# Kernel optimization log

Hardware: AMD Instinct MI355X
Metric: run time of the kernel (lower is better)

Reference implementation:

```python
import jax, jax.numpy as jnp
import numpy as np

EPS = 1e-6
ALPHA = 0.2  # LeakyReLU negative slope


def layer_norm(x, g, b):
    mu = jnp.mean(x, axis=-1, keepdims=True)
    var = jnp.mean(jnp.square(x - mu), axis=-1, keepdims=True)
    return (x - mu) * jax.lax.rsqrt(var + EPS) * g + b


def graph_attention(x, bias, W, a_src, a_dst):
    # x: [B,N,D], bias: [B,N,N], W: [D, H*Dh], a_src/a_dst: [H, Dh]
    B, N, D = x.shape
    H, Dh = a_src.shape
    h = jnp.einsum('bnd,dhk->bhnk', x, W.reshape(D, H, Dh))  # [B,H,N,Dh]
    s = jnp.einsum('bhnk,hk->bhn', h, a_src)                 # source term
    t = jnp.einsum('bhnk,hk->bhn', h, a_dst)                 # target term
    e = jax.nn.leaky_relu(s[:, :, :, None] + t[:, :, None, :], ALPHA)
    e = e + bias[:, None, :, :]                              # graph mask/bias
    attn = jax.nn.softmax(e, axis=-1)                        # [B,H,N,N]
    out = jnp.einsum('bhij,bhjk->bhik', attn, h)             # [B,H,N,Dh]
    return out.transpose(0, 2, 1, 3).reshape(B, N, H * Dh)


def setup_inputs() -> dict:
    key = jax.random.key(0)
    ks = jax.random.split(key, 8)
    B, N, D, H = 2, 2048, 512, 8
    Dh = D // H
    sc = 1.0 / np.sqrt(D)
    return {
        'x': jax.random.normal(ks[0], (B, N, D), jnp.float32),
        'bias': jax.random.normal(ks[1], (B, N, N), jnp.float32),
        'W1': jax.random.normal(ks[2], (D, D), jnp.float32) * sc,
        'a_src1': jax.random.normal(ks[3], (H, Dh), jnp.float32) * sc,
        'a_dst1': jax.random.normal(ks[4], (H, Dh), jnp.float32) * sc,
        'g1': jnp.ones((D,), jnp.float32),
        'b1': jnp.zeros((D,), jnp.float32),
        'W2': jax.random.normal(ks[5], (D, D), jnp.float32) * sc,
        'a_src2': jax.random.normal(ks[6], (1, D), jnp.float32) * sc,
        'a_dst2': jax.random.normal(ks[7], (1, D), jnp.float32) * sc,
        'g2': jnp.ones((D,), jnp.float32),
        'b2': jnp.zeros((D,), jnp.float32),
    }


def reference(x, bias, W1, a_src1, a_dst1, g1, b1, W2, a_src2, a_dst2, g2, b2):
    # dropout is identity in eval mode
    attn_in = layer_norm(x, g1, b1)
    attn = graph_attention(attn_in, bias, W1, a_src1, a_dst1) + x
    attn_in2 = layer_norm(attn, g2, b2)
    out = graph_attention(attn_in2, bias, W2, a_src2, a_dst2) + attn
    return out
```

## Files before the change

kernel.cpp:

```cpp
#include <hip/hip_runtime.h>
#include <math.h>

#define NB 2
#define NN 2048
#define DD 512
#define L2E 1.44269504088896340736f

typedef __attribute__((ext_vector_type(8))) short short8;
typedef __attribute__((ext_vector_type(4))) float f32x4;
typedef __attribute__((ext_vector_type(2))) float f32x2;

__device__ __forceinline__ unsigned short f2bf(float x) {
  union { float f; unsigned u; } a;
  a.f = x;
  unsigned r = a.u + 0x7FFF + ((a.u >> 16) & 1);
  return (unsigned short)(r >> 16);
}
__device__ __forceinline__ float bf2f(unsigned short u) {
  union { unsigned u; float f; } a;
  a.u = ((unsigned)u) << 16;
  return a.f;
}
__device__ __forceinline__ unsigned cvtpk(float lo, float hi) {
  unsigned r;
  asm("v_cvt_pk_bf16_f32 %0, %1, %2" : "=v"(r) : "v"(lo), "v"(hi));
  return r;
}
__device__ __forceinline__ uint2 exp4pk(float e0, float e1, float e2, float e3) {
  float p0, p1, p2, p3;
  uint2 d;
  asm("v_exp_f32 %2, %6\n\t"
      "v_exp_f32 %3, %7\n\t"
      "v_exp_f32 %4, %8\n\t"
      "v_exp_f32 %5, %9\n\t"
      "v_cvt_pk_bf16_f32 %0, %2, %3\n\t"
      "v_cvt_pk_bf16_f32 %1, %4, %5"
      : "=&v"(d.x), "=&v"(d.y), "=&v"(p0), "=&v"(p1), "=&v"(p2), "=&v"(p3)
      : "v"(e0), "v"(e1), "v"(e2), "v"(e3));
  return d;
}

__device__ __forceinline__ float waveReduceSum(float v) {
#pragma unroll
  for (int o = 32; o; o >>= 1) v += __shfl_down(v, o, 64);
  return v;
}
__device__ __forceinline__ float blockReduceSum(float v, float* red4) {
  int tid = threadIdx.x;
  __syncthreads();
  v = waveReduceSum(v);
  if ((tid & 63) == 0) red4[tid >> 6] = v;
  __syncthreads();
  return red4[0] + red4[1] + red4[2] + red4[3];
}

__global__ __launch_bounds__(256) void ln_kernel(const float* __restrict__ x,
                                                 const float* __restrict__ g,
                                                 const float* __restrict__ bb,
                                                 unsigned short* __restrict__ y) {
  int row = blockIdx.x;
  int t = threadIdx.x;
  const float* xr = x + (size_t)row * DD;
  __shared__ float red4[4];
  float2 v = *(const float2*)&xr[2 * t];
  float s = blockReduceSum(v.x + v.y, red4);
  float mu = s * (1.0f / 512.0f);
  float d0 = v.x - mu, d1 = v.y - mu;
  float ss = blockReduceSum(d0 * d0 + d1 * d1, red4);
  float rstd = rsqrtf(ss * (1.0f / 512.0f) + 1e-6f);
  float2 gg = *(const float2*)&g[2 * t];
  float2 bv = *(const float2*)&bb[2 * t];
  ushort2 o;
  o.x = f2bf(d0 * rstd * gg.x + bv.x);
  o.y = f2bf(d1 * rstd * gg.y + bv.y);
  *(ushort2*)&y[(size_t)row * DD + 2 * t] = o;
}

__global__ __launch_bounds__(256) void wt2_kernel(const float* __restrict__ W1,
                                                  const float* __restrict__ W2,
                                                  unsigned short* __restrict__ WT1,
                                                  unsigned short* __restrict__ WT2) {
  const float* W = blockIdx.z ? W2 : W1;
  unsigned short* WT = blockIdx.z ? WT2 : WT1;
  __shared__ float tile[64][65];
  int kt = blockIdx.x * 64, ct = blockIdx.y * 64;
  int t = threadIdx.x;
#pragma unroll
  for (int u = 0; u < 16; u++) {
    int lin = t + u * 256;
    int kl = lin >> 6, cl = lin & 63;
    tile[kl][cl] = W[(size_t)(kt + kl) * DD + ct + cl];
  }
  __syncthreads();
#pragma unroll
  for (int u = 0; u < 16; u++) {
    int lin = t + u * 256;
    int cl = lin >> 6, kl = lin & 63;
    WT[(size_t)(ct + cl) * DD + kt + kl] = f2bf(tile[kl][cl]);
  }
}

__global__ __launch_bounds__(256) void v2_kernel(
    const float* __restrict__ W1, const float* __restrict__ as1,
    const float* __restrict__ ad1, float* __restrict__ vs1, float* __restrict__ vd1,
    const float* __restrict__ W2, const float* __restrict__ as2,
    const float* __restrict__ ad2, float* __restrict__ vs2, float* __restrict__ vd2) {
  int slot = blockIdx.y;
  const float *W, *as, *ad;
  float *vs, *vd;
  int Dh, hoff;
  if (slot < 8) {
    W = W1; as = as1 + slot * 64; ad = ad1 + slot * 64;
    vs = vs1 + (size_t)slot * DD; vd = vd1 + (size_t)slot * DD;
    Dh = 64; hoff = slot * 64;
  } else {
    W = W2; as = as2; ad = ad2; vs = vs2; vd = vd2;
    Dh = 512; hoff = 0;
  }
  int t = threadIdx.x;
  int dl = t >> 2, kq = t & 3;
  int d = blockIdx.x * 64 + dl;
  int kn = Dh >> 2;
  const float* wr = W + (size_t)d * DD + hoff + kq * kn;
  const float* asp = as + kq * kn;
  const float* adp = ad + kq * kn;
  float s = 0.f, dd2 = 0.f;
  for (int k = 0; k < kn; k++) {
    float wv = wr[k];
    s += wv * asp[k];
    dd2 += wv * adp[k];
  }
  s += __shfl_xor(s, 1);
  s += __shfl_xor(s, 2);
  dd2 += __shfl_xor(dd2, 1);
  dd2 += __shfl_xor(dd2, 2);
  if (kq == 0) {
    vs[d] = s;
    vd[d] = dd2;
  }
}

__global__ __launch_bounds__(256) void biasH_kernel(const float* __restrict__ bias,
                                                    unsigned short* __restrict__ biasH) {
  int row = blockIdx.x;
  int t = threadIdx.x;
  const float* br = bias + (size_t)row * NN;
  float4 a = *(const float4*)&br[t * 4];
  float4 c = *(const float4*)&br[t * 4 + 1024];
  uint2 d0, d1;
  d0.x = cvtpk(a.x * L2E, a.y * L2E);
  d0.y = cvtpk(a.z * L2E, a.w * L2E);
  d1.x = cvtpk(c.x * L2E, c.y * L2E);
  d1.y = cvtpk(c.z * L2E, c.w * L2E);
  *(uint2*)&biasH[(size_t)row * NN + t * 4] = d0;
  *(uint2*)&biasH[(size_t)row * NN + t * 4 + 1024] = d1;
}

__global__ __launch_bounds__(256) void gemm_kernel(const unsigned short* __restrict__ A,
                                                   const unsigned short* __restrict__ BT,
                                                   unsigned short* __restrict__ hbT) {
  __shared__ float accL[4][16][65];
  int t = threadIdx.x, w = t >> 6, l = t & 63;
  int li = l & 15, lg = l >> 4;
  int R0 = blockIdx.x * 16;
  int c0 = blockIdx.y * 64;
  const unsigned short* ar = A + (size_t)(R0 + li) * DD + w * 128 + lg * 8;
  const unsigned short* br = BT + (size_t)(c0 + li) * DD + w * 128 + lg * 8;
  f32x4 acc[4] = {};
#pragma unroll
  for (int k0 = 0; k0 < 128; k0 += 32) {
    short8 af = *(const short8*)(ar + k0);
#pragma unroll
    for (int f = 0; f < 4; f++) {
      short8 bf = *(const short8*)(br + (size_t)f * 16 * DD + k0);
      acc[f] = __builtin_amdgcn_mfma_f32_16x16x32_bf16(af, bf, acc[f], 0, 0, 0);
    }
  }
#pragma unroll
  for (int f = 0; f < 4; f++)
#pragma unroll
    for (int r = 0; r < 4; r++) accL[w][lg * 4 + r][f * 16 + li] = acc[f][r];
  __syncthreads();
  int b = R0 >> 11, jT = (R0 & (NN - 1)) >> 4;
#pragma unroll
  for (int u = 0; u < 2; u++) {
    int idx = t + u * 256;
    int f = idx >> 7;
    int rem = idx & 127;
    int cl = rem >> 3, jlp = rem & 7;
    int cc = f * 16 + cl;
    float v0 = accL[0][2 * jlp][cc] + accL[1][2 * jlp][cc] + accL[2][2 * jlp][cc] +
               accL[3][2 * jlp][cc];
    float v1 = accL[0][2 * jlp + 1][cc] + accL[1][2 * jlp + 1][cc] +
               accL[2][2 * jlp + 1][cc] + accL[3][2 * jlp + 1][cc];
    size_t off = (((size_t)(b * (DD / 64) + blockIdx.y) * (NN / 16)) + jT) * 1024 +
                 f * 256 + cl * 16 + jlp * 2;
    *(unsigned*)(hbT + off) = cvtpk(v0, v1);
  }
}

__global__ __launch_bounds__(256) void st_kernel(const unsigned short* __restrict__ lnB,
                                                 const float* __restrict__ vs,
                                                 const float* __restrict__ vd,
                                                 float* __restrict__ sOut,
                                                 float* __restrict__ tOut, int HN) {
  int t = threadIdx.x, w = t >> 6, l = t & 63;
  int row = blockIdx.x * 4 + w;
  int b = row >> 11, n = row & (NN - 1);
  const unsigned short* lr = lnB + (size_t)row * DD + l * 8;
  union { short8 v; unsigned short u[8]; } xv;
  xv.v = *(const short8*)lr;
  float xf[8];
#pragma unroll
  for (int k = 0; k < 8; k++) xf[k] = bf2f(xv.u[k]);
  for (int h = 0; h < HN; h++) {
    const float* vsr = vs + (size_t)h * DD + l * 8;
    const float* vdr = vd + (size_t)h * DD + l * 8;
    float4 a0 = *(const float4*)vsr, a1 = *(const float4*)(vsr + 4);
    float4 c0 = *(const float4*)vdr, c1 = *(const float4*)(vdr + 4);
    float ps = xf[0] * a0.x + xf[1] * a0.y + xf[2] * a0.z + xf[3] * a0.w +
               xf[4] * a1.x + xf[5] * a1.y + xf[6] * a1.z + xf[7] * a1.w;
    float pd = xf[0] * c0.x + xf[1] * c0.y + xf[2] * c0.z + xf[3] * c0.w +
               xf[4] * c1.x + xf[5] * c1.y + xf[6] * c1.z + xf[7] * c1.w;
#pragma unroll
    for (int o = 32; o; o >>= 1) {
      ps += __shfl_xor(ps, o);
      pd += __shfl_xor(pd, o);
    }
    if (l == 0) {
      sOut[((size_t)b * HN + h) * NN + n] = ps * L2E;
      tOut[((size_t)b * HN + h) * NN + n] = pd * L2E;
    }
  }
}

template <int HN, int CCH>
__global__ __launch_bounds__(256) void pv_kernel(
    const unsigned short* __restrict__ hbT, const unsigned short* __restrict__ biasH,
    const float* __restrict__ sArr, const float* __restrict__ tArr,
    const float* __restrict__ res, float* __restrict__ out) {
  constexpr int DH = DD / HN;
  __shared__ unsigned short Pl[4][2][512];
  __shared__ float accL[4][16][33];
  __shared__ float sLa[4][16];
  int t = threadIdx.x, w = t >> 6, l = t & 63;
  int li = l & 15, lg = l >> 4;
  int i0 = blockIdx.x * 16;
  int ck = blockIdx.y, bh = blockIdx.z;
  int h = bh % HN, b = bh / HN;
  int c0 = h * DH + ck * (CCH * 64);
  size_t bhN = (size_t)bh * NN;
  const float* trow = tArr + bhN;

  int rs = l >> 3;
  int js = (l & 7) * 4;
  int wq = (((l & 7) >> 1) ^ (rs & 3)) * 8 + (l & 1) * 4;
  float sv[2];
  sv[0] = sArr[bhN + i0 + rs];
  sv[1] = sArr[bhN + i0 + 8 + rs];
  const unsigned short* bb0 = biasH + ((size_t)b * NN + i0 + rs) * NN;
  const unsigned short* bb1 = bb0 + (size_t)8 * NN;

  const unsigned short* vbase =
      hbT + ((size_t)(b * (DD / 64) + (c0 >> 6)) * (NN / 16)) * 1024 +
      (lg >> 1) * 1024 + li * 16 + (lg & 1) * 8;
  int ra0 = li * 32 + ((lg ^ (li & 3)) * 8);

  union { short8 v; unsigned short q[8]; } ones;
#pragma unroll
  for (int k = 0; k < 8; k++) ones.q[k] = 0x3F80;

  const int jbeg = w * (NN / 4), jend = jbeg + NN / 4;
  f32x4 acc[CCH][4] = {};
  f32x4 accS = {0.f, 0.f, 0.f, 0.f};

  auto loadTB = [&](int j, float4& tv, uint2& q0, uint2& q1) {
    tv = *(const float4*)&trow[j + js];
    q0 = *(const uint2*)&bb0[j + js];
    q1 = *(const uint2*)&bb1[j + js];
  };
  auto loadV = [&](int j, short8 (&vv)[CCH][4]) {
#pragma unroll
    for (int cc = 0; cc < CCH; cc++) {
      const unsigned short* vp =
          vbase + (size_t)cc * ((NN / 16) * 1024) + (size_t)j * 64;
#pragma unroll
      for (int f = 0; f < 4; f++) vv[cc][f] = *(const short8*)(vp + f * 256);
    }
  };
  auto computeP = [&](const float4& tv, uint2 q0, uint2 q1, int pb) {
    f32x2 t01 = {tv.x, tv.y}, t23 = {tv.z, tv.w};
#pragma unroll
    for (int u = 0; u < 2; u++) {
      uint2 qu = u ? q1 : q0;
      int row = u * 8 + rs;
      f32x2 s2 = {sv[u], sv[u]};
      f32x2 e01 = s2 + t01, e23 = s2 + t23;
      e01 = __builtin_elementwise_max(e01, e01 * 0.2f);
      e23 = __builtin_elementwise_max(e23, e23 * 0.2f);
      f32x2 b01 = {__uint_as_float(qu.x << 16), __uint_as_float(qu.x & 0xFFFF0000u)};
      f32x2 b23 = {__uint_as_float(qu.y << 16), __uint_as_float(qu.y & 0xFFFF0000u)};
      e01 += b01;
      e23 += b23;
      uint2 d = exp4pk(e01.x, e01.y, e23.x, e23.y);
      *(uint2*)&Pl[w][pb][row * 32 + wq] = d;
    }
  };
  auto domfma = [&](short8 a0, const short8 (&vv)[CCH][4]) {
    __builtin_amdgcn_s_setprio(1);
    accS = __builtin_amdgcn_mfma_f32_16x16x32_bf16(a0, ones.v, accS, 0, 0, 0);
#pragma unroll
    for (int cc = 0; cc < CCH; cc++)
#pragma unroll
      for (int f = 0; f < 4; f++)
        acc[cc][f] =
            __builtin_amdgcn_mfma_f32_16x16x32_bf16(a0, vv[cc][f], acc[cc][f], 0, 0, 0);
    __builtin_amdgcn_s_setprio(0);
  };

  float4 tvA, tvB;
  uint2 qA0, qA1, qB0, qB1;
  short8 vA[CCH][4], vB[CCH][4];

  loadTB(jbeg, tvA, qA0, qA1);
  computeP(tvA, qA0, qA1, 0);
  loadTB(jbeg + 32, tvA, qA0, qA1);
  loadV(jbeg, vA);

  for (int jt = jbeg; jt < jend; jt += 64) {
    short8 a0 = *(const short8*)&Pl[w][0][ra0];
    loadV(jt + 32, vB);
    loadTB(jt + 64, tvB, qB0, qB1);
    computeP(tvA, qA0, qA1, 1);
    domfma(a0, vA);
    short8 a1 = *(const short8*)&Pl[w][1][ra0];
    if (jt + 64 < jend) {
      loadV(jt + 64, vA);
      loadTB(jt + 96, tvA, qA0, qA1);
      computeP(tvB, qB0, qB1, 0);
    }
    domfma(a1, vB);
  }

  if (li == 0) {
#pragma unroll
    for (int r = 0; r < 4; r++) sLa[w][lg * 4 + r] = accS[r];
  }
#pragma unroll
  for (int g = 0; g < 2 * CCH; g++) {
    int cc = g >> 1, half = g & 1;
#pragma unroll
    for (int f = 0; f < 2; f++)
#pragma unroll
      for (int r = 0; r < 4; r++)
        accL[w][lg * 4 + r][f * 16 + li] = acc[cc][half * 2 + f][r];
    __syncthreads();
    {
      int rr = t >> 4, cp = (t & 15) * 2;
      float S = sLa[0][rr] + sLa[1][rr] + sLa[2][rr] + sLa[3][rr];
      float inv = 1.0f / S;
      float2 O = {0.f, 0.f};
#pragma unroll
      for (int w2 = 0; w2 < 4; w2++) {
        O.x += accL[w2][rr][cp];
        O.y += accL[w2][rr][cp + 1];
      }
      size_t ix = ((size_t)b * NN + i0 + rr) * DD + c0 + cc * 64 + half * 32 + cp;
      float2 rv = *(const float2*)&res[ix];
      float2 ov = {O.x * inv + rv.x, O.y * inv + rv.y};
      *(float2*)&out[ix] = ov;
    }
    __syncthreads();
  }
}

extern "C" void kernel_launch(void* const* d_in, const int* in_sizes, int n_in,
                              void* d_out, int out_size, void* d_ws, size_t ws_size,
                              hipStream_t stream) {
  const float* x = (const float*)d_in[0];
  const float* bias = (const float*)d_in[1];
  const float* W1 = (const float*)d_in[2];
  const float* asrc1 = (const float*)d_in[3];
  const float* adst1 = (const float*)d_in[4];
  const float* g1 = (const float*)d_in[5];
  const float* b1 = (const float*)d_in[6];
  const float* W2 = (const float*)d_in[7];
  const float* asrc2 = (const float*)d_in[8];
  const float* adst2 = (const float*)d_in[9];
  const float* g2 = (const float*)d_in[10];
  const float* b2 = (const float*)d_in[11];
  float* out = (float*)d_out;
  float* ws = (float*)d_ws;

  const size_t RC = (size_t)NB * NN * DD;
  float* attnBuf = ws;
  unsigned short* lnB = (unsigned short*)(ws + RC);
  unsigned short* hbT = (unsigned short*)(ws + RC + RC / 2);
  unsigned short* WT1 = (unsigned short*)(ws + 2 * RC);
  unsigned short* WT2 = WT1 + (size_t)DD * DD;
  float* vs1 = (float*)(WT2 + (size_t)DD * DD);
  float* vd1 = vs1 + 8 * DD;
  float* vs2 = vd1 + 8 * DD;
  float* vd2 = vs2 + DD;
  float* sBuf = vd2 + DD;
  float* tBuf = sBuf + 16 * NN;
  unsigned short* biasH = (unsigned short*)(tBuf + 16 * NN);

  const int rows = NB * NN;

  hipLaunchKernelGGL(wt2_kernel, dim3(8, 8, 2), dim3(256), 0, stream, W1, W2, WT1, WT2);
  hipLaunchKernelGGL(v2_kernel, dim3(8, 9), dim3(256), 0, stream, W1, asrc1, adst1, vs1, vd1,
                     W2, asrc2, adst2, vs2, vd2);
  hipLaunchKernelGGL(biasH_kernel, dim3(rows), dim3(256), 0, stream, bias, biasH);

  hipLaunchKernelGGL(ln_kernel, dim3(rows), dim3(256), 0, stream, x, g1, b1, lnB);
  hipLaunchKernelGGL(gemm_kernel, dim3(256, 8), dim3(256), 0, stream, lnB, WT1, hbT);
  hipLaunchKernelGGL(st_kernel, dim3(rows / 4), dim3(256), 0, stream, lnB, vs1, vd1, sBuf, tBuf, 8);
  hipLaunchKernelGGL((pv_kernel<8, 1>), dim3(128, 1, 16), dim3(256), 0, stream, hbT, biasH,
                     sBuf, tBuf, x, attnBuf);

  hipLaunchKernelGGL(ln_kernel, dim3(rows), dim3(256), 0, stream, attnBuf, g2, b2, lnB);
  hipLaunchKernelGGL(gemm_kernel, dim3(256, 8), dim3(256), 0, stream, lnB, WT2, hbT);
  hipLaunchKernelGGL(st_kernel, dim3(rows / 4), dim3(256), 0, stream, lnB, vs2, vd2, sBuf, tBuf, 1);
  hipLaunchKernelGGL((pv_kernel<1, 2>), dim3(128, 4, 2), dim3(256), 0, stream, hbT, biasH,
                     sBuf, tBuf, attnBuf, out);
}
```

Measured before the change: 165.9 us.

## Merge prep kernels, fuse LN with score projections, widen PV tiles

Three preprocessing kernels (bias conversion, weight transpose, attention vector projection) are folded into one launch that dispatches on block index. LayerNorm is fused with the s/t score computation, so scores are taken from fp32 LN output kept in shared memory instead of re-reading the bf16 buffer. The PV attention kernel is restructured to handle 64 keys per step with wider 8-element loads and a single V register set consumed by two MFMA passes, replacing the previous 32-key A/B ping-pong. These changes cut launch count and global traffic, but the PV rework changes register pressure and the overlap of loads with compute. Scores now use fp32 rather than bf16-rounded LN values, which slightly alters the numerics.

```diff
diff --git a/kernel.cpp b/kernel.cpp
--- a/kernel.cpp
+++ b/kernel.cpp
@@ -8,7 +8,6 @@
 
 typedef __attribute__((ext_vector_type(8))) short short8;
 typedef __attribute__((ext_vector_type(4))) float f32x4;
-typedef __attribute__((ext_vector_type(2))) float f32x2;
 
 __device__ __forceinline__ unsigned short f2bf(float x) {
   union { float f; unsigned u; } a;
@@ -54,14 +53,94 @@
   return red4[0] + red4[1] + red4[2] + red4[3];
 }
 
-__global__ __launch_bounds__(256) void ln_kernel(const float* __restrict__ x,
-                                                 const float* __restrict__ g,
-                                                 const float* __restrict__ bb,
-                                                 unsigned short* __restrict__ y) {
+__global__ __launch_bounds__(256) void prep_kernel(
+    const float* __restrict__ bias, unsigned short* __restrict__ biasH,
+    const float* __restrict__ W1, const float* __restrict__ W2,
+    unsigned short* __restrict__ WT1, unsigned short* __restrict__ WT2,
+    const float* __restrict__ as1, const float* __restrict__ ad1,
+    float* __restrict__ vs1, float* __restrict__ vd1,
+    const float* __restrict__ as2, const float* __restrict__ ad2,
+    float* __restrict__ vs2, float* __restrict__ vd2) {
+  __shared__ float tile[64][65];
+  int bid = blockIdx.x;
+  int t = threadIdx.x;
+  if (bid < 4096) {
+    const float* br = bias + (size_t)bid * NN;
+    float4 a = *(const float4*)&br[t * 4];
+    float4 c = *(const float4*)&br[t * 4 + 1024];
+    uint2 d0, d1;
+    d0.x = cvtpk(a.x * L2E, a.y * L2E);
+    d0.y = cvtpk(a.z * L2E, a.w * L2E);
+    d1.x = cvtpk(c.x * L2E, c.y * L2E);
+    d1.y = cvtpk(c.z * L2E, c.w * L2E);
+    *(uint2*)&biasH[(size_t)bid * NN + t * 4] = d0;
+    *(uint2*)&biasH[(size_t)bid * NN + t * 4 + 1024] = d1;
+  } else if (bid < 4096 + 128) {
+    int idx = bid - 4096;
+    const float* W = (idx & 64) ? W2 : W1;
+    unsigned short* WT = (idx & 64) ? WT2 : WT1;
+    int r = idx & 63;
+    int kt = (r >> 3) * 64, ct = (r & 7) * 64;
+#pragma unroll
+    for (int u = 0; u < 16; u++) {
+      int lin = t + u * 256;
+      int kl = lin >> 6, cl = lin & 63;
+      tile[kl][cl] = W[(size_t)(kt + kl) * DD + ct + cl];
+    }
+    __syncthreads();
+#pragma unroll
+    for (int u = 0; u < 16; u++) {
+      int lin = t + u * 256;
+      int cl = lin >> 6, kl = lin & 63;
+      WT[(size_t)(ct + cl) * DD + kt + kl] = f2bf(tile[kl][cl]);
+    }
+  } else {
+    int idx = bid - 4224;
+    int slot = idx >> 3, dch = idx & 7;
+    const float *W, *as, *ad;
+    float *vs, *vd;
+    int Dh, hoff;
+    if (slot < 8) {
+      W = W1; as = as1 + slot * 64; ad = ad1 + slot * 64;
+      vs = vs1 + (size_t)slot * DD; vd = vd1 + (size_t)slot * DD;
+      Dh = 64; hoff = slot * 64;
+    } else {
+      W = W2; as = as2; ad = ad2; vs = vs2; vd = vd2;
+      Dh = 512; hoff = 0;
+    }
+    int dl = t >> 2, kq = t & 3;
+    int d = dch * 64 + dl;
+    int kn = Dh >> 2;
+    const float* wr = W + (size_t)d * DD + hoff + kq * kn;
+    const float* asp = as + kq * kn;
+    const float* adp = ad + kq * kn;
+    float s = 0.f, dd2 = 0.f;
+    for (int k = 0; k < kn; k++) {
+      float wv = wr[k];
+      s += wv * asp[k];
+      dd2 += wv * adp[k];
+    }
+    s += __shfl_xor(s, 1);
+    s += __shfl_xor(s, 2);
+    dd2 += __shfl_xor(dd2, 1);
+    dd2 += __shfl_xor(dd2, 2);
+    if (kq == 0) {
+      vs[d] = s;
+      vd[d] = dd2;
+    }
+  }
+}
+
+__global__ __launch_bounds__(256) void lnst_kernel(
+    const float* __restrict__ x, const float* __restrict__ g,
+    const float* __restrict__ bb, unsigned short* __restrict__ y,
+    const float* __restrict__ vs, const float* __restrict__ vd,
+    float* __restrict__ sOut, float* __restrict__ tOut, int HN) {
+  __shared__ float red4[4];
+  __shared__ float lnS[512];
   int row = blockIdx.x;
   int t = threadIdx.x;
   const float* xr = x + (size_t)row * DD;
-  __shared__ float red4[4];
   float2 v = *(const float2*)&xr[2 * t];
   float s = blockReduceSum(v.x + v.y, red4);
   float mu = s * (1.0f / 512.0f);
@@ -70,90 +149,38 @@
   float rstd = rsqrtf(ss * (1.0f / 512.0f) + 1e-6f);
   float2 gg = *(const float2*)&g[2 * t];
   float2 bv = *(const float2*)&bb[2 * t];
+  float n0 = d0 * rstd * gg.x + bv.x;
+  float n1 = d1 * rstd * gg.y + bv.y;
   ushort2 o;
-  o.x = f2bf(d0 * rstd * gg.x + bv.x);
-  o.y = f2bf(d1 * rstd * gg.y + bv.y);
+  o.x = f2bf(n0);
+  o.y = f2bf(n1);
   *(ushort2*)&y[(size_t)row * DD + 2 * t] = o;
-}
-
-__global__ __launch_bounds__(256) void wt2_kernel(const float* __restrict__ W1,
-                                                  const float* __restrict__ W2,
-                                                  unsigned short* __restrict__ WT1,
-                                                  unsigned short* __restrict__ WT2) {
-  const float* W = blockIdx.z ? W2 : W1;
-  unsigned short* WT = blockIdx.z ? WT2 : WT1;
-  __shared__ float tile[64][65];
-  int kt = blockIdx.x * 64, ct = blockIdx.y * 64;
-  int t = threadIdx.x;
-#pragma unroll
-  for (int u = 0; u < 16; u++) {
-    int lin = t + u * 256;
-    int kl = lin >> 6, cl = lin & 63;
-    tile[kl][cl] = W[(size_t)(kt + kl) * DD + ct + cl];
-  }
+  lnS[2 * t] = n0;
+  lnS[2 * t + 1] = n1;
   __syncthreads();
-#pragma unroll
-  for (int u = 0; u < 16; u++) {
-    int lin = t + u * 256;
-    int cl = lin >> 6, kl = lin & 63;
-    WT[(size_t)(ct + cl) * DD + kt + kl] = f2bf(tile[kl][cl]);
-  }
-}
-
-__global__ __launch_bounds__(256) void v2_kernel(
-    const float* __restrict__ W1, const float* __restrict__ as1,
-    const float* __restrict__ ad1, float* __restrict__ vs1, float* __restrict__ vd1,
-    const float* __restrict__ W2, const float* __restrict__ as2,
-    const float* __restrict__ ad2, float* __restrict__ vs2, float* __restrict__ vd2) {
-  int slot = blockIdx.y;
-  const float *W, *as, *ad;
-  float *vs, *vd;
-  int Dh, hoff;
-  if (slot < 8) {
-    W = W1; as = as1 + slot * 64; ad = ad1 + slot * 64;
-    vs = vs1 + (size_t)slot * DD; vd = vd1 + (size_t)slot * DD;
-    Dh = 64; hoff = slot * 64;
-  } else {
-    W = W2; as = as2; ad = ad2; vs = vs2; vd = vd2;
-    Dh = 512; hoff = 0;
-  }
-  int t = threadIdx.x;
-  int dl = t >> 2, kq = t & 3;
-  int d = blockIdx.x * 64 + dl;
-  int kn = Dh >> 2;
-  const float* wr = W + (size_t)d * DD + hoff + kq * kn;
-  const float* asp = as + kq * kn;
-  const float* adp = ad + kq * kn;
-  float s = 0.f, dd2 = 0.f;
-  for (int k = 0; k < kn; k++) {
-    float wv = wr[k];
-    s += wv * asp[k];
-    dd2 += wv * adp[k];
-  }
-  s += __shfl_xor(s, 1);
-  s += __shfl_xor(s, 2);
-  dd2 += __shfl_xor(dd2, 1);
-  dd2 += __shfl_xor(dd2, 2);
-  if (kq == 0) {
-    vs[d] = s;
-    vd[d] = dd2;
-  }
-}
-
-__global__ __launch_bounds__(256) void biasH_kernel(const float* __restrict__ bias,
-                                                    unsigned short* __restrict__ biasH) {
-  int row = blockIdx.x;
-  int t = threadIdx.x;
-  const float* br = bias + (size_t)row * NN;
-  float4 a = *(const float4*)&br[t * 4];
-  float4 c = *(const float4*)&br[t * 4 + 1024];
-  uint2 d0, d1;
-  d0.x = cvtpk(a.x * L2E, a.y * L2E);
-  d0.y = cvtpk(a.z * L2E, a.w * L2E);
-  d1.x = cvtpk(c.x * L2E, c.y * L2E);
-  d1.y = cvtpk(c.z * L2E, c.w * L2E);
-  *(uint2*)&biasH[(size_t)row * NN + t * 4] = d0;
-  *(uint2*)&biasH[(size_t)row * NN + t * 4 + 1024] = d1;
+  int wv = t >> 6, l = t & 63;
+  int b = row >> 11, n = row & (NN - 1);
+  float4 x0 = *(const float4*)&lnS[l * 8];
+  float4 x1 = *(const float4*)&lnS[l * 8 + 4];
+  for (int h = wv; h < HN; h += 4) {
+    const float* vsr = vs + (size_t)h * DD + l * 8;
+    const float* vdr = vd + (size_t)h * DD + l * 8;
+    float4 a0 = *(const float4*)vsr, a1 = *(const float4*)(vsr + 4);
+    float4 c0 = *(const float4*)vdr, c1 = *(const float4*)(vdr + 4);
+    float ps = x0.x * a0.x + x0.y * a0.y + x0.z * a0.z + x0.w * a0.w +
+               x1.x * a1.x + x1.y * a1.y + x1.z * a1.z + x1.w * a1.w;
+    float pd = x0.x * c0.x + x0.y * c0.y + x0.z * c0.z + x0.w * c0.w +
+               x1.x * c1.x + x1.y * c1.y + x1.z * c1.z + x1.w * c1.w;
+#pragma unroll
+    for (int o2 = 32; o2; o2 >>= 1) {
+      ps += __shfl_xor(ps, o2);
+      pd += __shfl_xor(pd, o2);
+    }
+    if (l == 0) {
+      sOut[((size_t)b * HN + h) * NN + n] = ps * L2E;
+      tOut[((size_t)b * HN + h) * NN + n] = pd * L2E;
+    }
+  }
 }
 
 __global__ __launch_bounds__(256) void gemm_kernel(const unsigned short* __restrict__ A,
@@ -199,48 +226,13 @@
   }
 }
 
-__global__ __launch_bounds__(256) void st_kernel(const unsigned short* __restrict__ lnB,
-                                                 const float* __restrict__ vs,
-                                                 const float* __restrict__ vd,
-                                                 float* __restrict__ sOut,
-                                                 float* __restrict__ tOut, int HN) {
-  int t = threadIdx.x, w = t >> 6, l = t & 63;
-  int row = blockIdx.x * 4 + w;
-  int b = row >> 11, n = row & (NN - 1);
-  const unsigned short* lr = lnB + (size_t)row * DD + l * 8;
-  union { short8 v; unsigned short u[8]; } xv;
-  xv.v = *(const short8*)lr;
-  float xf[8];
-#pragma unroll
-  for (int k = 0; k < 8; k++) xf[k] = bf2f(xv.u[k]);
-  for (int h = 0; h < HN; h++) {
-    const float* vsr = vs + (size_t)h * DD + l * 8;
-    const float* vdr = vd + (size_t)h * DD + l * 8;
-    float4 a0 = *(const float4*)vsr, a1 = *(const float4*)(vsr + 4);
-    float4 c0 = *(const float4*)vdr, c1 = *(const float4*)(vdr + 4);
-    float ps = xf[0] * a0.x + xf[1] * a0.y + xf[2] * a0.z + xf[3] * a0.w +
-               xf[4] * a1.x + xf[5] * a1.y + xf[6] * a1.z + xf[7] * a1.w;
-    float pd = xf[0] * c0.x + xf[1] * c0.y + xf[2] * c0.z + xf[3] * c0.w +
-               xf[4] * c1.x + xf[5] * c1.y + xf[6] * c1.z + xf[7] * c1.w;
-#pragma unroll
-    for (int o = 32; o; o >>= 1) {
-      ps += __shfl_xor(ps, o);
-      pd += __shfl_xor(pd, o);
-    }
-    if (l == 0) {
-      sOut[((size_t)b * HN + h) * NN + n] = ps * L2E;
-      tOut[((size_t)b * HN + h) * NN + n] = pd * L2E;
-    }
-  }
-}
-
 template <int HN, int CCH>
 __global__ __launch_bounds__(256) void pv_kernel(
     const unsigned short* __restrict__ hbT, const unsigned short* __restrict__ biasH,
     const float* __restrict__ sArr, const float* __restrict__ tArr,
     const float* __restrict__ res, float* __restrict__ out) {
   constexpr int DH = DD / HN;
-  __shared__ unsigned short Pl[4][2][512];
+  __shared__ unsigned short Pl[4][2][1024];
   __shared__ float accL[4][16][33];
   __shared__ float sLa[4][16];
   int t = threadIdx.x, w = t >> 6, l = t & 63;
@@ -253,8 +245,9 @@
   const float* trow = tArr + bhN;
 
   int rs = l >> 3;
-  int js = (l & 7) * 4;
-  int wq = (((l & 7) >> 1) ^ (rs & 3)) * 8 + (l & 1) * 4;
+  int js = (l & 7) * 8;
+  int jc = l & 7;
+  int wchunk = ((jc & 4) | ((jc & 3) ^ (rs & 3))) * 8;
   float sv[2];
   sv[0] = sArr[bhN + i0 + rs];
   sv[1] = sArr[bhN + i0 + 8 + rs];
@@ -264,7 +257,8 @@
   const unsigned short* vbase =
       hbT + ((size_t)(b * (DD / 64) + (c0 >> 6)) * (NN / 16)) * 1024 +
       (lg >> 1) * 1024 + li * 16 + (lg & 1) * 8;
-  int ra0 = li * 32 + ((lg ^ (li & 3)) * 8);
+  int ra0 = li * 64 + ((lg ^ (li & 3))) * 8;
+  int ra1 = ra0 + 32;
 
   union { short8 v; unsigned short q[8]; } ones;
 #pragma unroll
@@ -274,39 +268,49 @@
   f32x4 acc[CCH][4] = {};
   f32x4 accS = {0.f, 0.f, 0.f, 0.f};
 
-  auto loadTB = [&](int j, float4& tv, uint2& q0, uint2& q1) {
-    tv = *(const float4*)&trow[j + js];
-    q0 = *(const uint2*)&bb0[j + js];
-    q1 = *(const uint2*)&bb1[j + js];
+  auto loadTB = [&](int j, float4& t0, float4& t1, uint4& q0, uint4& q1) {
+    t0 = *(const float4*)&trow[j + js];
+    t1 = *(const float4*)&trow[j + js + 4];
+    q0 = *(const uint4*)&bb0[j + js];
+    q1 = *(const uint4*)&bb1[j + js];
   };
-  auto loadV = [&](int j, short8 (&vv)[CCH][4]) {
+  auto computeP = [&](const float4& t0, const float4& t1, uint4 q0, uint4 q1, int pb) {
+#pragma unroll
+    for (int u = 0; u < 2; u++) {
+      uint4 qu = u ? q1 : q0;
+      int row = u * 8 + rs;
+      float e0 = sv[u] + t0.x, e1 = sv[u] + t0.y;
+      float e2 = sv[u] + t0.z, e3 = sv[u] + t0.w;
+      float e4 = sv[u] + t1.x, e5 = sv[u] + t1.y;
+      float e6 = sv[u] + t1.z, e7 = sv[u] + t1.w;
+      e0 = fmaxf(e0, 0.2f * e0) + __uint_as_float(qu.x << 16);
+      e1 = fmaxf(e1, 0.2f * e1) + __uint_as_float(qu.x & 0xFFFF0000u);
+      e2 = fmaxf(e2, 0.2f * e2) + __uint_as_float(qu.y << 16);
+      e3 = fmaxf(e3, 0.2f * e3) + __uint_as_float(qu.y & 0xFFFF0000u);
+      e4 = fmaxf(e4, 0.2f * e4) + __uint_as_float(qu.z << 16);
+      e5 = fmaxf(e5, 0.2f * e5) + __uint_as_float(qu.z & 0xFFFF0000u);
+      e6 = fmaxf(e6, 0.2f * e6) + __uint_as_float(qu.w << 16);
+      e7 = fmaxf(e7, 0.2f * e7) + __uint_as_float(qu.w & 0xFFFF0000u);
+      uint2 d0 = exp4pk(e0, e1, e2, e3);
+      uint2 d1 = exp4pk(e4, e5, e6, e7);
+      uint4 dd;
+      dd.x = d0.x; dd.y = d0.y; dd.z = d1.x; dd.w = d1.y;
+      *(uint4*)&Pl[w][pb][row * 64 + wchunk] = dd;
+    }
+  };
+  auto loadV = [&](int jt, short8 (&vv)[CCH][8]) {
 #pragma unroll
     for (int cc = 0; cc < CCH; cc++) {
       const unsigned short* vp =
-          vbase + (size_t)cc * ((NN / 16) * 1024) + (size_t)j * 64;
-#pragma unroll
-      for (int f = 0; f < 4; f++) vv[cc][f] = *(const short8*)(vp + f * 256);
+          vbase + (size_t)cc * ((NN / 16) * 1024) + (size_t)jt * 64;
+#pragma unroll
+      for (int f = 0; f < 4; f++) {
+        vv[cc][f] = *(const short8*)(vp + f * 256);
+        vv[cc][4 + f] = *(const short8*)(vp + 2048 + f * 256);
+      }
     }
   };
-  auto computeP = [&](const float4& tv, uint2 q0, uint2 q1, int pb) {
-    f32x2 t01 = {tv.x, tv.y}, t23 = {tv.z, tv.w};
-#pragma unroll
-    for (int u = 0; u < 2; u++) {
-      uint2 qu = u ? q1 : q0;
-      int row = u * 8 + rs;
-      f32x2 s2 = {sv[u], sv[u]};
-      f32x2 e01 = s2 + t01, e23 = s2 + t23;
-      e01 = __builtin_elementwise_max(e01, e01 * 0.2f);
-      e23 = __builtin_elementwise_max(e23, e23 * 0.2f);
-      f32x2 b01 = {__uint_as_float(qu.x << 16), __uint_as_float(qu.x & 0xFFFF0000u)};
-      f32x2 b23 = {__uint_as_float(qu.y << 16), __uint_as_float(qu.y & 0xFFFF0000u)};
-      e01 += b01;
-      e23 += b23;
-      uint2 d = exp4pk(e01.x, e01.y, e23.x, e23.y);
-      *(uint2*)&Pl[w][pb][row * 32 + wq] = d;
-    }
-  };
-  auto domfma = [&](short8 a0, const short8 (&vv)[CCH][4]) {
+  auto domfma = [&](short8 a0, short8 a1, const short8 (&vv)[CCH][8]) {
     __builtin_amdgcn_s_setprio(1);
     accS = __builtin_amdgcn_mfma_f32_16x16x32_bf16(a0, ones.v, accS, 0, 0, 0);
 #pragma unroll
@@ -315,31 +319,37 @@
       for (int f = 0; f < 4; f++)
         acc[cc][f] =
             __builtin_amdgcn_mfma_f32_16x16x32_bf16(a0, vv[cc][f], acc[cc][f], 0, 0, 0);
+    accS = __builtin_amdgcn_mfma_f32_16x16x32_bf16(a1, ones.v, accS, 0, 0, 0);
+#pragma unroll
+    for (int cc = 0; cc < CCH; cc++)
+#pragma unroll
+      for (int f = 0; f < 4; f++)
+        acc[cc][f] =
+            __builtin_amdgcn_mfma_f32_16x16x32_bf16(a1, vv[cc][4 + f], acc[cc][f], 0, 0, 0);
     __builtin_amdgcn_s_setprio(0);
   };
 
-  float4 tvA, tvB;
-  uint2 qA0, qA1, qB0, qB1;
-  short8 vA[CCH][4], vB[CCH][4];
-
-  loadTB(jbeg, tvA, qA0, qA1);
-  computeP(tvA, qA0, qA1, 0);
-  loadTB(jbeg + 32, tvA, qA0, qA1);
-  loadV(jbeg, vA);
-
+  float4 tA0, tA1;
+  uint4 qA0, qA1;
+  short8 vv[CCH][8];
+
+  loadTB(jbeg, tA0, tA1, qA0, qA1);
+  computeP(tA0, tA1, qA0, qA1, 0);
+  loadTB(jbeg + 64, tA0, tA1, qA0, qA1);
+
+  int buf = 0;
   for (int jt = jbeg; jt < jend; jt += 64) {
-    short8 a0 = *(const short8*)&Pl[w][0][ra0];
-    loadV(jt + 32, vB);
-    loadTB(jt + 64, tvB, qB0, qB1);
-    computeP(tvA, qA0, qA1, 1);
-    domfma(a0, vA);
-    short8 a1 = *(const short8*)&Pl[w][1][ra0];
+    loadV(jt, vv);
+    short8 a0 = *(const short8*)&Pl[w][buf][ra0];
+    short8 a1 = *(const short8*)&Pl[w][buf][ra1];
     if (jt + 64 < jend) {
-      loadV(jt + 64, vA);
-      loadTB(jt + 96, tvA, qA0, qA1);
-      computeP(tvB, qB0, qB1, 0);
-    }
-    domfma(a1, vB);
+      float4 n0 = tA0, n1 = tA1;
+      uint4 m0 = qA0, m1 = qA1;
+      loadTB(jt + 128, tA0, tA1, qA0, qA1);
+      computeP(n0, n1, m0, m1, buf ^ 1);
+    }
+    domfma(a0, a1, vv);
+    buf ^= 1;
   }
 
   if (li == 0) {
@@ -408,20 +418,18 @@
 
   const int rows = NB * NN;
 
-  hipLaunchKernelGGL(wt2_kernel, dim3(8, 8, 2), dim3(256), 0, stream, W1, W2, WT1, WT2);
-  hipLaunchKernelGGL(v2_kernel, dim3(8, 9), dim3(256), 0, stream, W1, asrc1, adst1, vs1, vd1,
-                     W2, asrc2, adst2, vs2, vd2);
-  hipLaunchKernelGGL(biasH_kernel, dim3(rows), dim3(256), 0, stream, bias, biasH);
-
-  hipLaunchKernelGGL(ln_kernel, dim3(rows), dim3(256), 0, stream, x, g1, b1, lnB);
+  hipLaunchKernelGGL(prep_kernel, dim3(4096 + 128 + 72), dim3(256), 0, stream, bias, biasH,
+                     W1, W2, WT1, WT2, asrc1, adst1, vs1, vd1, asrc2, adst2, vs2, vd2);
+
+  hipLaunchKernelGGL(lnst_kernel, dim3(rows), dim3(256), 0, stream, x, g1, b1, lnB, vs1, vd1,
+                     sBuf, tBuf, 8);
   hipLaunchKernelGGL(gemm_kernel, dim3(256, 8), dim3(256), 0, stream, lnB, WT1, hbT);
-  hipLaunchKernelGGL(st_kernel, dim3(rows / 4), dim3(256), 0, stream, lnB, vs1, vd1, sBuf, tBuf, 8);
   hipLaunchKernelGGL((pv_kernel<8, 1>), dim3(128, 1, 16), dim3(256), 0, stream, hbT, biasH,
                      sBuf, tBuf, x, attnBuf);
 
-  hipLaunchKernelGGL(ln_kernel, dim3(rows), dim3(256), 0, stream, attnBuf, g2, b2, lnB);
+  hipLaunchKernelGGL(lnst_kernel, dim3(rows), dim3(256), 0, stream, attnBuf, g2, b2, lnB, vs2,
+                     vd2, sBuf, tBuf, 1);
   hipLaunchKernelGGL(gemm_kernel, dim3(256, 8), dim3(256), 0, stream, lnB, WT2, hbT);
-  hipLaunchKernelGGL(st_kernel, dim3(rows / 4), dim3(256), 0, stream, lnB, vs2, vd2, sBuf, tBuf, 1);
   hipLaunchKernelGGL((pv_kernel<1, 2>), dim3(128, 4, 2), dim3(256), 0, stream, hbT, biasH,
                      sBuf, tBuf, attnBuf, out);
 }
```

Result: faster. 154.2 us (-7.0%).
